# Optimization experiments

Hardware: AMD Instinct MI355X
Metric: run time of the kernel (lower is better)

The kernel has to match this reference:

```python
import jax, jax.numpy as jnp
import numpy as np

K_NBR = 64          # max_num_neighbors in radius()
RATIO1, R1 = 0.5, 0.2
RATIO2, R2 = 0.25, 0.4


def _mlp(h, params):
    # PyG MLP: Linear+ReLU per hidden layer, plain last layer (BN is identity at
    # init / eval with fresh running stats, so omitted).
    for w, b in params[:-1]:
        h = jax.nn.relu(h @ w + b)
    w, b = params[-1]
    return h @ w + b


def _fps(pos, S):
    # Farthest point sampling, deterministic start at index 0. pos: [N,3]
    min_d = jnp.sum((pos - pos[0]) ** 2, axis=-1)

    def body(md, _):
        i = jnp.argmax(md)
        md = jnp.minimum(md, jnp.sum((pos - pos[i]) ** 2, axis=-1))
        return md, i

    _, idxs = jax.lax.scan(body, min_d, None, length=S - 1)
    return jnp.concatenate([jnp.zeros((1,), idxs.dtype), idxs])  # [S]


def _sa(x, pos, S, r, params):
    # One SAModule for a single cloud. x: [N,C], pos: [N,3]
    sel = _fps(pos, S)
    pos_s = pos[sel]                                                   # [S,3]
    d2 = jnp.sum((pos_s[:, None, :] - pos[None, :, :]) ** 2, axis=-1)  # [S,N]
    score = jnp.where(d2 <= r * r, -d2, -jnp.inf)
    vals, nbr = jax.lax.top_k(score, K_NBR)      # <=64 nearest within radius r
    mask = vals > -jnp.inf                       # [S,K]; center always valid
    # PointNetConv message: cat([x_j, pos_j - pos_i]) -> local MLP -> max-aggr
    feats = jnp.concatenate([x[nbr], pos[nbr] - pos_s[:, None, :]], axis=-1)
    h = _mlp(feats, params)                      # [S,K,Cout]
    h = jnp.max(jnp.where(mask[..., None], h, -jnp.inf), axis=1)
    return h, pos_s


def _forward(data, p1, p2, p3, fc_w, fc_b):
    B, N, _ = data.shape
    S1 = int(np.ceil(N * RATIO1))
    S2 = int(np.ceil(S1 * RATIO2))
    # sa1 is called with x = pos = raw coordinates
    x1, pos1 = jax.vmap(lambda p: _sa(p, p, S1, R1, p1))(data)
    x2, pos2 = jax.vmap(lambda x, p: _sa(x, p, S2, R2, p2))(x1, pos1)
    # GlobalSAModule: MLP on cat([x, pos]) then global max pool per cloud
    g = jnp.max(_mlp(jnp.concatenate([x2, pos2], axis=-1), p3), axis=1)  # [B,1024]
    return g @ fc_w + fc_b


def setup_inputs() -> dict:
    key = jax.random.key(0)
    ks = jax.random.split(key, 16)
    B, N = 4, 4096
    inp = {"data": jax.random.uniform(ks[0], (B, N, 3), jnp.float32)}
    dims = {"sa1": [6, 64, 64, 128],
            "sa2": [131, 128, 128, 256],
            "sa3": [259, 256, 512, 1024]}
    i = 1
    for name, ds in dims.items():
        for l in range(len(ds) - 1):
            fi, fo = ds[l], ds[l + 1]
            inp[f"{name}_w{l + 1}"] = (jax.random.normal(ks[i], (fi, fo), jnp.float32)
                                       / np.float32(np.sqrt(fi)))
            inp[f"{name}_b{l + 1}"] = jnp.zeros((fo,), jnp.float32)
            i += 1
    inp["fc_w"] = jax.random.normal(ks[i], (1024, 256), jnp.float32) / np.float32(32.0)
    inp["fc_b"] = jnp.zeros((256,), jnp.float32)
    return inp


def reference(data, sa1_w1, sa1_b1, sa1_w2, sa1_b2, sa1_w3, sa1_b3,
              sa2_w1, sa2_b1, sa2_w2, sa2_b2, sa2_w3, sa2_b3,
              sa3_w1, sa3_b1, sa3_w2, sa3_b2, sa3_w3, sa3_b3,
              fc_w, fc_b):
    p1 = [(sa1_w1, sa1_b1), (sa1_w2, sa1_b2), (sa1_w3, sa1_b3)]
    p2 = [(sa2_w1, sa2_b1), (sa2_w2, sa2_b2), (sa2_w3, sa2_b3)]
    p3 = [(sa3_w1, sa3_b1), (sa3_w2, sa3_b2), (sa3_w3, sa3_b3)]
    return _forward(data, p1, p2, p3, fc_w, fc_b)  # [B, 256]
```

## Files before the change

### kernel.cpp

```cpp
#include <hip/hip_runtime.h>


#define DEVFN __device__ __forceinline__

DEVFN float d2_exact(float ax, float ay, float az, float bx, float by, float bz) {
    float dx = __fsub_rn(ax, bx);
    float dy = __fsub_rn(ay, by);
    float dz = __fsub_rn(az, bz);
    return __fadd_rn(__fadd_rn(__fmul_rn(dx, dx), __fmul_rn(dy, dy)), __fmul_rn(dz, dz));
}

DEVFN unsigned long long u64max(unsigned long long a, unsigned long long b) {
    return a > b ? a : b;
}

template <int R>
DEVFN unsigned long long dpp_ror16_u64(unsigned long long x) {
    int lo = (int)(unsigned)(x & 0xFFFFFFFFull);
    int hi = (int)(unsigned)(x >> 32);
    lo = __builtin_amdgcn_update_dpp(lo, lo, 0x120 | R, 0xF, 0xF, false);
    hi = __builtin_amdgcn_update_dpp(hi, hi, 0x120 | R, 0xF, 0xF, false);
    return ((unsigned long long)(unsigned)hi << 32) | (unsigned)lo;
}

DEVFN unsigned long long rl_u64(unsigned long long x, int lane) {
    unsigned l = (unsigned)__builtin_amdgcn_readlane((int)(unsigned)(x & 0xFFFFFFFFull), lane);
    unsigned h = (unsigned)__builtin_amdgcn_readlane((int)(unsigned)(x >> 32), lane);
    return ((unsigned long long)h << 32) | l;
}

template <int N, int S, int NT>
DEVFN void run_fps(const float* sx, const float* sy, const float* sz,
                   unsigned long long* sPack,
                   int* selLds) {
    constexpr int PPT = N / NT;
    constexpr int NW = NT / 64;
    const int tid = threadIdx.x;
    float px[PPT], py[PPT], pz[PPT], md[PPT];
    unsigned loc[PPT];
#pragma unroll
    for (int i = 0; i < PPT; ++i) {
        int idx = tid * PPT + i;
        px[i] = sx[idx]; py[i] = sy[idx]; pz[i] = sz[idx];
        md[i] = __builtin_inff();
        loc[i] = 0xFFFFFFFFu - (unsigned)idx;
    }
    if (tid == 0) selLds[0] = 0;
    int cur = 0;
    for (int s = 1; s < S; ++s) {
        float ax = sx[cur], ay = sy[cur], az = sz[cur];
        unsigned long long tq[PPT];
#pragma unroll
        for (int i = 0; i < PPT; ++i) {
            float d = d2_exact(px[i], py[i], pz[i], ax, ay, az);
            float m = fminf(md[i], d);
            md[i] = m;
            tq[i] = ((unsigned long long)__float_as_uint(m) << 32) |
                    (unsigned long long)loc[i];
        }
#pragma unroll
        for (int w = PPT / 2; w >= 1; w >>= 1)
#pragma unroll
            for (int i = 0; i < w; ++i) tq[i] = u64max(tq[i], tq[i + w]);

        unsigned long long pk = tq[0];
        pk = u64max(pk, dpp_ror16_u64<8>(pk));
        pk = u64max(pk, dpp_ror16_u64<4>(pk));
        pk = u64max(pk, dpp_ror16_u64<2>(pk));
        pk = u64max(pk, dpp_ror16_u64<1>(pk));

        unsigned long long wmax = u64max(u64max(rl_u64(pk, 0), rl_u64(pk, 16)),
                                         u64max(rl_u64(pk, 32), rl_u64(pk, 48)));

        unsigned long long* sp = sPack + (s & 1) * NW;
        if ((tid & 63) == 0) sp[tid >> 6] = wmax;
        __syncthreads();

        unsigned long long win;
        if constexpr (NW == 8) {
            const ulonglong2* sp2 = (const ulonglong2*)sp;
            ulonglong2 q0 = sp2[0], q1 = sp2[1], q2 = sp2[2], q3 = sp2[3];
            unsigned long long m01 = u64max(u64max(q0.x, q0.y), u64max(q1.x, q1.y));
            unsigned long long m23 = u64max(u64max(q2.x, q2.y), u64max(q3.x, q3.y));
            win = u64max(m01, m23);
        } else {
            const ulonglong2* sp2 = (const ulonglong2*)sp;
            ulonglong2 q0 = sp2[0], q1 = sp2[1];
            win = u64max(u64max(q0.x, q0.y), u64max(q1.x, q1.y));
        }

        cur = (int)(0xFFFFFFFFu - (unsigned)(win & 0xFFFFFFFFull));
        if (tid == 0) selLds[s] = cur;
    }
}

template <int N, int CAP>
DEVFN void nbr_body(const float* __restrict__ pos,
                    const float cx, const float cy, const float cz,
                    const float rsq, const int c,
                    int* __restrict__ nbr, int* __restrict__ cnt,
                    float* sDw, int* sIw) {
    const int lane = threadIdx.x & 63;
    int count = 0;
    for (int j = lane; j < N; j += 64) {
        float d = d2_exact(cx, cy, cz, pos[j * 3 + 0], pos[j * 3 + 1], pos[j * 3 + 2]);
        bool pred = (d <= rsq);
        unsigned long long m = __ballot(pred);
        int wpos = count + __popcll(m & ((1ull << lane) - 1ull));
        if (pred && wpos < CAP) { sDw[wpos] = d; sIw[wpos] = j; }
        count += __popcll(m);
    }
    if (count > CAP) count = CAP;

    for (int t = lane; t < count; t += 64) {
        float d = sDw[t]; int id = sIw[t];
        int rank = 0;
        int j0 = 0;
        for (; j0 + 4 <= count; j0 += 4) {
            float4 dj = *(const float4*)&sDw[j0];
            int4   ij = *(const int4*)&sIw[j0];
            rank += (dj.x < d || (dj.x == d && ij.x < id)) ? 1 : 0;
            rank += (dj.y < d || (dj.y == d && ij.y < id)) ? 1 : 0;
            rank += (dj.z < d || (dj.z == d && ij.z < id)) ? 1 : 0;
            rank += (dj.w < d || (dj.w == d && ij.w < id)) ? 1 : 0;
        }
        for (; j0 < count; ++j0) {
            float dj = sDw[j0]; int ij = sIw[j0];
            rank += (dj < d || (dj == d && ij < id)) ? 1 : 0;
        }
        if (rank < 64) nbr[(size_t)c * 64 + rank] = id;
    }
    if (lane == 0) cnt[c] = count < 64 ? count : 64;
}

__global__ __launch_bounds__(512) void fpsnbr_kernel(
    const float* __restrict__ data,
    float* __restrict__ mdG,
    int* __restrict__ selG,
    float* __restrict__ pos1,
    const int sb, const int se,
    const float rsq, int* __restrict__ nbr1, int* __restrict__ cnt1,
    const int s0)
{
    __shared__ __align__(16) char raw[65536];
    const int tid = threadIdx.x;

    if (blockIdx.x >= 4) {
        float* sD = (float*)raw;
        int*   sI = (int*)(raw + 32768);
        const int wid = tid >> 6;
        const int g = (int)(blockIdx.x - 4) * 8 + wid;
        const int b = g >> 9;
        const int s = s0 + (g & 511);
        const int c = b * 2048 + s;
        const float cx = pos1[(size_t)c * 3 + 0];
        const float cy = pos1[(size_t)c * 3 + 1];
        const float cz = pos1[(size_t)c * 3 + 2];
        nbr_body<4096, 1024>(data + (size_t)b * 4096 * 3, cx, cy, cz, rsq, c,
                             nbr1, cnt1, sD + wid * 1024, sI + wid * 1024);
        return;
    }

    constexpr int N = 4096, NT = 512, PPT = N / NT, NW = NT / 64;
    float* sx = (float*)raw;
    float* sy = sx + 4096;
    float* sz = sy + 4096;
    unsigned long long* sPack = (unsigned long long*)(raw + 49152);
    int* sSel = (int*)(raw + 49280);

    const int b = blockIdx.x;
    const float* p = data + (size_t)b * N * 3;
    for (int i = tid; i < N; i += NT) {
        sx[i] = p[i * 3 + 0]; sy[i] = p[i * 3 + 1]; sz[i] = p[i * 3 + 2];
    }
    __syncthreads();

    float px[PPT], py[PPT], pz[PPT], md[PPT];
    const bool first = (sb == 1);
#pragma unroll
    for (int i = 0; i < PPT; ++i) {
        int idx = tid * PPT + i;
        px[i] = sx[idx]; py[i] = sy[idx]; pz[i] = sz[idx];
        md[i] = first ? __builtin_inff() : mdG[(size_t)b * N + idx];
    }
    int cur = first ? 0 : selG[(size_t)b * 2048 + sb - 1];
    if (first && tid == 0) selG[(size_t)b * 2048] = 0;
    const unsigned lob = 0xFFFFFFFFu - (unsigned)(tid * PPT);

    for (int s = sb; s < se; ++s) {
        float ax = sx[cur], ay = sy[cur], az = sz[cur];
        float mm[PPT];
#pragma unroll
        for (int i = 0; i < PPT; ++i) {
            float d = d2_exact(px[i], py[i], pz[i], ax, ay, az);
            float m = fminf(md[i], d);
            md[i] = m; mm[i] = m;
        }
        float a0 = fmaxf(mm[0], mm[4]), a1 = fmaxf(mm[1], mm[5]);
        float a2 = fmaxf(mm[2], mm[6]), a3 = fmaxf(mm[3], mm[7]);
        float b0 = fmaxf(a0, a2), b1 = fmaxf(a1, a3);
        float mloc = fmaxf(b0, b1);
        int li = 7;
#pragma unroll
        for (int i = 6; i >= 0; --i) li = (mm[i] == mloc) ? i : li;

        unsigned long long k0 =
            ((unsigned long long)__float_as_uint(mloc) << 32) |
            (unsigned long long)(lob - (unsigned)li);

        k0 = u64max(k0, dpp_ror16_u64<8>(k0));
        k0 = u64max(k0, dpp_ror16_u64<4>(k0));
        k0 = u64max(k0, dpp_ror16_u64<2>(k0));
        k0 = u64max(k0, dpp_ror16_u64<1>(k0));

        unsigned long long wmax = u64max(u64max(rl_u64(k0, 0), rl_u64(k0, 16)),
                                         u64max(rl_u64(k0, 32), rl_u64(k0, 48)));

        unsigned long long* sp = sPack + (s & 1) * NW;
        if ((tid & 63) == 0) sp[tid >> 6] = wmax;
        __syncthreads();

        const ulonglong2* sp2 = (const ulonglong2*)sp;
        ulonglong2 q0 = sp2[0], q1 = sp2[1], q2 = sp2[2], q3 = sp2[3];
        unsigned long long m01 = u64max(u64max(q0.x, q0.y), u64max(q1.x, q1.y));
        unsigned long long m23 = u64max(u64max(q2.x, q2.y), u64max(q3.x, q3.y));
        unsigned long long win = u64max(m01, m23);

        cur = (int)(0xFFFFFFFFu - (unsigned)(win & 0xFFFFFFFFull));
        if (tid == 0) sSel[s - sb] = cur;
    }
    __syncthreads();

    if (se < 2048) {
#pragma unroll
        for (int i = 0; i < PPT; ++i)
            mdG[(size_t)b * N + tid * PPT + i] = md[i];
    }
    if (tid == 0) selG[(size_t)b * 2048 + se - 1] = cur;

    float* p1 = pos1 + (size_t)b * 2048 * 3;
    const int sb0 = first ? 0 : sb;
    for (int s = sb0 + tid; s < se; s += NT) {
        int idx = (s == 0) ? 0 : sSel[s - sb];
        p1[s * 3 + 0] = sx[idx]; p1[s * 3 + 1] = sy[idx]; p1[s * 3 + 2] = sz[idx];
    }
}

__global__ __launch_bounds__(512) void fps2nbr_kernel(
    const float* __restrict__ data,
    const float* __restrict__ pos1,
    float* __restrict__ pos2,
    const float rsq, int* __restrict__ nbr1, int* __restrict__ cnt1,
    const int s0)
{
    __shared__ __align__(16) char raw[65536];
    const int tid = threadIdx.x;

    if (blockIdx.x >= 4) {
        float* sD = (float*)raw;
        int*   sI = (int*)(raw + 32768);
        const int wid = tid >> 6;
        const int g = (int)(blockIdx.x - 4) * 8 + wid;
        const int b = g >> 9;
        const int s = s0 + (g & 511);
        const int c = b * 2048 + s;
        const float cx = pos1[(size_t)c * 3 + 0];
        const float cy = pos1[(size_t)c * 3 + 1];
        const float cz = pos1[(size_t)c * 3 + 2];
        nbr_body<4096, 1024>(data + (size_t)b * 4096 * 3, cx, cy, cz, rsq, c,
                             nbr1, cnt1, sD + wid * 1024, sI + wid * 1024);
        return;
    }

    float* sx = (float*)raw;
    float* sy = sx + 2048;
    float* sz = sy + 2048;
    int* sSel2 = (int*)(raw + 24576);
    unsigned long long* sPack2 = (unsigned long long*)(raw + 26624);

    const int b = blockIdx.x;
    const float* p1 = pos1 + (size_t)b * 2048 * 3;
    for (int i = tid; i < 2048; i += 512) {
        sx[i] = p1[i * 3 + 0]; sy[i] = p1[i * 3 + 1]; sz[i] = p1[i * 3 + 2];
    }
    __syncthreads();

    run_fps<2048, 512, 512>(sx, sy, sz, sPack2, sSel2);
    __syncthreads();

    float* p2 = pos2 + (size_t)b * 512 * 3;
    {
        int si = sSel2[tid];
        p2[tid * 3 + 0] = sx[si]; p2[tid * 3 + 1] = sy[si]; p2[tid * 3 + 2] = sz[si];
    }
}

DEVFN void tile44_fma(const float* __restrict__ aBase, int aStride,
                      const float* __restrict__ wBase, int wStride,
                      int nk4, float (&acc)[4][4]) {
    for (int k4 = 0; k4 < nk4; ++k4) {
        float a[4][4], w[4][4];
#pragma unroll
        for (int i = 0; i < 4; ++i) {
            float4 t = *(const float4*)(aBase + i * aStride + k4 * 4);
            a[i][0] = t.x; a[i][1] = t.y; a[i][2] = t.z; a[i][3] = t.w;
        }
#pragma unroll
        for (int kk = 0; kk < 4; ++kk) {
            float4 t = *(const float4*)(wBase + (size_t)(k4 * 4 + kk) * wStride);
            w[kk][0] = t.x; w[kk][1] = t.y; w[kk][2] = t.z; w[kk][3] = t.w;
        }
#pragma unroll
        for (int kk = 0; kk < 4; ++kk)
#pragma unroll
            for (int i = 0; i < 4; ++i)
#pragma unroll
                for (int j = 0; j < 4; ++j)
                    acc[i][j] = fmaf(a[i][kk], w[kk][j], acc[i][j]);
    }
}

DEVFN void tile48_fma(const float* __restrict__ aBase, int aStride,
                      const float* __restrict__ wBase, int wStride,
                      int nk4, float (&acc)[4][8]) {
    for (int k4 = 0; k4 < nk4; ++k4) {
        float a[4][4];
#pragma unroll
        for (int i = 0; i < 4; ++i) {
            float4 t = *(const float4*)(aBase + i * aStride + k4 * 4);
            a[i][0] = t.x; a[i][1] = t.y; a[i][2] = t.z; a[i][3] = t.w;
        }
#pragma unroll
        for (int kk = 0; kk < 4; ++kk) {
            float4 t0 = *(const float4*)(wBase + (size_t)(k4 * 4 + kk) * wStride);
            float4 t1 = *(const float4*)(wBase + (size_t)(k4 * 4 + kk) * wStride + 4);
            float w_[8] = {t0.x, t0.y, t0.z, t0.w, t1.x, t1.y, t1.z, t1.w};
#pragma unroll
            for (int i = 0; i < 4; ++i)
#pragma unroll
                for (int j = 0; j < 8; ++j)
                    acc[i][j] = fmaf(a[i][kk], w_[j], acc[i][j]);
        }
    }
}

__global__ __launch_bounds__(256) void mlp1nbr2_kernel(
    const float* __restrict__ pos,
    const float* __restrict__ ctr,
    const int* __restrict__ nbr, const int* __restrict__ cnt,
    const float* __restrict__ w1, const float* __restrict__ b1,
    const float* __restrict__ w2, const float* __restrict__ b2,
    const float* __restrict__ w3, const float* __restrict__ b3,
    float* __restrict__ x1,
    const float* __restrict__ pos1,
    const float* __restrict__ pos2,
    const float rsq2, int* __restrict__ nbr2, int* __restrict__ cnt2)
{
    __shared__ __align__(16) float smem[12288];
    const int tid = threadIdx.x;

    if (blockIdx.x < 512) {
        float* sD = smem;
        int*   sI = (int*)(smem + 6144);
        const int wid = tid >> 6;
        const int c = (int)blockIdx.x * 4 + wid;
        const int b = c >> 9;
        const float cx = pos2[(size_t)c * 3 + 0];
        const float cy = pos2[(size_t)c * 3 + 1];
        const float cz = pos2[(size_t)c * 3 + 2];
        nbr_body<2048, 1536>(pos1 + (size_t)b * 2048 * 3, cx, cy, cz, rsq2, c,
                             nbr2, cnt2, sD + wid * 1536, sI + wid * 1536);
        return;
    }

    float* sFeat = smem;
    float* sH1   = smem + 576;
    float* sH2   = smem + 4928;
    float* sRed  = smem + 9280;

    const int c = blockIdx.x - 512;
    const int b = c >> 11;
    const int valid = cnt[c];

    if (tid < 64) {
        const int r = tid;
        float fx = 0.f, fy = 0.f, fz = 0.f, dx = 0.f, dy = 0.f, dz = 0.f;
        if (r < valid) {
            int j = nbr[(size_t)c * 64 + r];
            const float* pj = pos + ((size_t)b * 4096 + j) * 3;
            fx = pj[0]; fy = pj[1]; fz = pj[2];
            dx = fx - ctr[c * 3 + 0]; dy = fy - ctr[c * 3 + 1]; dz = fz - ctr[c * 3 + 2];
        }
        float* fr = sFeat + r * 9;
        fr[0] = fx; fr[1] = fy; fr[2] = fz; fr[3] = dx; fr[4] = dy; fr[5] = dz;
    }
    __syncthreads();

    {
        const int r = tid & 63, c0 = (tid >> 6) * 16;
        float acc[16];
#pragma unroll
        for (int q = 0; q < 16; ++q) acc[q] = b1[c0 + q];
#pragma unroll
        for (int k = 0; k < 6; ++k) {
            float a = sFeat[r * 9 + k];
#pragma unroll
            for (int q = 0; q < 16; ++q) acc[q] = fmaf(a, w1[k * 64 + c0 + q], acc[q]);
        }
        float* hr = sH1 + r * 68 + c0;
#pragma unroll
        for (int q = 0; q < 16; ++q) hr[q] = fmaxf(acc[q], 0.f);
    }
    __syncthreads();

    {
        const int r0 = (tid >> 4) * 4, c0 = (tid & 15) * 4;
        float acc[4][4];
#pragma unroll
        for (int i = 0; i < 4; ++i)
#pragma unroll
            for (int j = 0; j < 4; ++j) acc[i][j] = b2[c0 + j];
        tile44_fma(sH1 + r0 * 68, 68, w2 + c0, 64, 16, acc);
#pragma unroll
        for (int i = 0; i < 4; ++i)
#pragma unroll
            for (int j = 0; j < 4; ++j)
                sH2[(r0 + i) * 68 + c0 + j] = fmaxf(acc[i][j], 0.f);
    }
    __syncthreads();

    {
        const int r0 = (tid >> 4) * 4, c0 = (tid & 15) * 8;
        float acc[4][8];
#pragma unroll
        for (int i = 0; i < 4; ++i)
#pragma unroll
            for (int j = 0; j < 8; ++j) acc[i][j] = 0.f;
        tile48_fma(sH2 + r0 * 68, 68, w3 + c0, 128, 16, acc);
        float pm[8];
#pragma unroll
        for (int j = 0; j < 8; ++j) pm[j] = -__builtin_inff();
#pragma unroll
        for (int i = 0; i < 4; ++i)
            if (r0 + i < valid)
#pragma unroll
                for (int j = 0; j < 8; ++j) pm[j] = fmaxf(pm[j], acc[i][j]);
#pragma unroll
        for (int j = 0; j < 8; ++j) sRed[(tid >> 4) * 128 + c0 + j] = pm[j];
    }
    __syncthreads();
    if (tid < 128) {
        float m = -__builtin_inff();
#pragma unroll
        for (int g = 0; g < 16; ++g) m = fmaxf(m, sRed[g * 128 + tid]);
        x1[(size_t)c * 128 + tid] = m + b3[tid];
    }
}

__global__ __launch_bounds__(512, 4) void mlp2_kernel(
    const float* __restrict__ x1,
    const float* __restrict__ pos1,
    const float* __restrict__ ctr,
    const int* __restrict__ nbr, const int* __restrict__ cnt,
    const float* __restrict__ w1, const float* __restrict__ b1,
    const float* __restrict__ w2, const float* __restrict__ b2,
    const float* __restrict__ w3, const float* __restrict__ b3,
    float* __restrict__ x2)
{
    __shared__ __align__(16) float sF[64 * 132];
    __shared__ __align__(16) float sH[64 * 132];
    float* sRed = sH;

    const int tid = threadIdx.x;
    const int c = blockIdx.x;
    const int b = c >> 9;
    const int valid = cnt[c];
    const float cx = ctr[c * 3 + 0], cy = ctr[c * 3 + 1], cz = ctr[c * 3 + 2];

    {
        const int r = tid >> 3, t8 = tid & 7;
        float* fr = sF + r * 132;
        if (r < valid) {
            int j = nbr[(size_t)c * 64 + r];
            const float* xp = x1 + ((size_t)b * 2048 + j) * 128;
#pragma unroll
            for (int q = 0; q < 4; ++q) {
                float4 v = *(const float4*)(xp + t8 * 16 + q * 4);
                fr[t8 * 16 + q * 4 + 0] = v.x; fr[t8 * 16 + q * 4 + 1] = v.y;
                fr[t8 * 16 + q * 4 + 2] = v.z; fr[t8 * 16 + q * 4 + 3] = v.w;
            }
            if (t8 == 0) {
                const float* pj = pos1 + ((size_t)b * 2048 + j) * 3;
                fr[128] = pj[0] - cx; fr[129] = pj[1] - cy; fr[130] = pj[2] - cz;
                fr[131] = 0.f;
            }
        } else {
#pragma unroll
            for (int q = 0; q < 16; ++q) fr[t8 * 16 + q] = 0.f;
            if (t8 == 0) { fr[128] = 0.f; fr[129] = 0.f; fr[130] = 0.f; fr[131] = 0.f; }
        }
    }
    __syncthreads();

    const int r0 = (tid >> 5) * 4;
    const int c0 = (tid & 31) * 4;
    const int c8 = (tid & 31) * 8;

    {
        float acc[4][4];
#pragma unroll
        for (int i = 0; i < 4; ++i)
#pragma unroll
            for (int j = 0; j < 4; ++j) acc[i][j] = b1[c0 + j];
        tile44_fma(sF + r0 * 132, 132, w1 + c0, 128, 32, acc);
        for (int k = 128; k < 131; ++k) {
            float4 wv = *(const float4*)(w1 + (size_t)k * 128 + c0);
            float w_[4] = {wv.x, wv.y, wv.z, wv.w};
#pragma unroll
            for (int i = 0; i < 4; ++i) {
                float a = sF[(r0 + i) * 132 + k];
#pragma unroll
                for (int j = 0; j < 4; ++j) acc[i][j] = fmaf(a, w_[j], acc[i][j]);
            }
        }
#pragma unroll
        for (int i = 0; i < 4; ++i)
#pragma unroll
            for (int j = 0; j < 4; ++j)
                sH[(r0 + i) * 132 + c0 + j] = fmaxf(acc[i][j], 0.f);
    }
    __syncthreads();

    {
        float acc[4][4];
#pragma unroll
        for (int i = 0; i < 4; ++i)
#pragma unroll
            for (int j = 0; j < 4; ++j) acc[i][j] = b2[c0 + j];
        tile44_fma(sH + r0 * 132, 132, w2 + c0, 128, 32, acc);
#pragma unroll
        for (int i = 0; i < 4; ++i)
#pragma unroll
            for (int j = 0; j < 4; ++j)
                sF[(r0 + i) * 132 + c0 + j] = fmaxf(acc[i][j], 0.f);
    }
    __syncthreads();

    {
        float acc[4][8];
#pragma unroll
        for (int i = 0; i < 4; ++i)
#pragma unroll
            for (int j = 0; j < 8; ++j) acc[i][j] = 0.f;
        tile48_fma(sF + r0 * 132, 132, w3 + c8, 256, 32, acc);
        float pm[8];
#pragma unroll
        for (int j = 0; j < 8; ++j) pm[j] = -__builtin_inff();
#pragma unroll
        for (int i = 0; i < 4; ++i)
            if (r0 + i < valid)
#pragma unroll
                for (int j = 0; j < 8; ++j) pm[j] = fmaxf(pm[j], acc[i][j]);
#pragma unroll
        for (int j = 0; j < 8; ++j) sRed[(tid >> 5) * 256 + c8 + j] = pm[j];
    }
    __syncthreads();
    if (tid < 256) {
        float m = -__builtin_inff();
#pragma unroll
        for (int g = 0; g < 16; ++g) m = fmaxf(m, sRed[g * 256 + tid]);
        x2[(size_t)c * 256 + tid] = m + b3[tid];
    }
}

__global__ __launch_bounds__(256) void gemm1f_kernel(const float* __restrict__ x2,
                                                     const float* __restrict__ pos2,
                                                     const float* __restrict__ W,
                                                     const float* __restrict__ bias,
                                                     float* __restrict__ C) {
    constexpr int K = 259, Nc = 256;
    __shared__ __align__(16) float sA[64 * 36];
    __shared__ __align__(16) float sB[32 * 68];
    const int tid = threadIdx.x;
    const int row0 = blockIdx.y * 64, col0 = blockIdx.x * 64;
    const int r0 = (tid >> 4) * 4, c0 = (tid & 15) * 4;
    float acc[4][4];
#pragma unroll
    for (int i = 0; i < 4; ++i)
#pragma unroll
        for (int j = 0; j < 4; ++j) acc[i][j] = 0.f;

    for (int kb = 0; kb < K; kb += 32) {
        for (int l = tid; l < 64 * 32; l += 256) {
            int r = l >> 5, k = l & 31;
            int gk = kb + k;
            float av = 0.f;
            if (gk < K) {
                int row = row0 + r;
                av = (gk < 256) ? x2[(size_t)row * 256 + gk]
                                : pos2[row * 3 + (gk - 256)];
            }
            sA[r * 36 + k] = av;
        }
        for (int l = tid; l < 32 * 64; l += 256) {
            int k = l >> 6, cc = l & 63;
            sB[k * 68 + cc] = (kb + k < K) ? W[(size_t)(kb + k) * Nc + col0 + cc] : 0.f;
        }
        __syncthreads();
        tile44_fma(sA + r0 * 36, 36, sB + c0, 68, 8, acc);
        __syncthreads();
    }
#pragma unroll
    for (int i = 0; i < 4; ++i)
#pragma unroll
        for (int j = 0; j < 4; ++j)
            C[(size_t)(row0 + r0 + i) * Nc + col0 + c0 + j] =
                fmaxf(acc[i][j] + bias[col0 + c0 + j], 0.f);
}

__global__ __launch_bounds__(256) void gemm_kernel(const float* __restrict__ A,
                                                   const float* __restrict__ W,
                                                   const float* __restrict__ bias,
                                                   float* __restrict__ C,
                                                   int M, int K, int Nc, int relu) {
    __shared__ __align__(16) float sA[64 * 36];
    __shared__ __align__(16) float sB[32 * 68];
    const int tid = threadIdx.x;
    const int row0 = blockIdx.y * 64, col0 = blockIdx.x * 64;
    const int r0 = (tid >> 4) * 4, c0 = (tid & 15) * 4;
    float acc[4][4];
#pragma unroll
    for (int i = 0; i < 4; ++i)
#pragma unroll
        for (int j = 0; j < 4; ++j) acc[i][j] = 0.f;

    for (int kb = 0; kb < K; kb += 32) {
        for (int l = tid; l < 64 * 32; l += 256) {
            int r = l >> 5, k = l & 31;
            sA[r * 36 + k] = (kb + k < K) ? A[(size_t)(row0 + r) * K + kb + k] : 0.f;
        }
        for (int l = tid; l < 32 * 64; l += 256) {
            int k = l >> 6, cc = l & 63;
            sB[k * 68 + cc] = (kb + k < K) ? W[(size_t)(kb + k) * Nc + col0 + cc] : 0.f;
        }
        __syncthreads();
        tile44_fma(sA + r0 * 36, 36, sB + c0, 68, 8, acc);
        __syncthreads();
    }
#pragma unroll
    for (int i = 0; i < 4; ++i)
#pragma unroll
        for (int j = 0; j < 4; ++j) {
            float v = acc[i][j] + bias[col0 + c0 + j];
            if (relu) v = fmaxf(v, 0.f);
            C[(size_t)(row0 + r0 + i) * Nc + col0 + c0 + j] = v;
        }
}

__global__ __launch_bounds__(1024) void mpfc_kernel(const float* __restrict__ h,
                                                    const float* __restrict__ w,
                                                    const float* __restrict__ bias,
                                                    float* __restrict__ out) {
    __shared__ float sG[1024];
    __shared__ float sP[4][256];
    const int b = blockIdx.x, tid = threadIdx.x;

    float m = -__builtin_inff();
    const float* hp = h + (size_t)b * 512 * 1024 + tid;
    for (int r = 0; r < 512; ++r) m = fmaxf(m, hp[(size_t)r * 1024]);
    sG[tid] = m;
    __syncthreads();

    const int c = tid & 255, kc = tid >> 8;
    float acc = 0.f;
    const float* wp = w + (size_t)(kc * 256) * 256 + c;
    const float* gp = sG + kc * 256;
    for (int k = 0; k < 256; ++k) acc = fmaf(gp[k], wp[(size_t)k * 256], acc);
    sP[kc][c] = acc;
    __syncthreads();
    if (tid < 256)
        out[b * 256 + tid] = ((sP[0][tid] + sP[1][tid]) + (sP[2][tid] + sP[3][tid]))
                             + bias[tid];
}

extern "C" void kernel_launch(void* const* d_in, const int* in_sizes, int n_in,
                              void* d_out, int out_size, void* d_ws, size_t ws_size,
                              hipStream_t stream) {
    const float* data  = (const float*)d_in[0];
    const float* s1w1  = (const float*)d_in[1];
    const float* s1b1  = (const float*)d_in[2];
    const float* s1w2  = (const float*)d_in[3];
    const float* s1b2  = (const float*)d_in[4];
    const float* s1w3  = (const float*)d_in[5];
    const float* s1b3  = (const float*)d_in[6];
    const float* s2w1  = (const float*)d_in[7];
    const float* s2b1  = (const float*)d_in[8];
    const float* s2w2  = (const float*)d_in[9];
    const float* s2b2  = (const float*)d_in[10];
    const float* s2w3  = (const float*)d_in[11];
    const float* s2b3  = (const float*)d_in[12];
    const float* s3w1  = (const float*)d_in[13];
    const float* s3b1  = (const float*)d_in[14];
    const float* s3w2  = (const float*)d_in[15];
    const float* s3b2  = (const float*)d_in[16];
    const float* s3w3  = (const float*)d_in[17];
    const float* s3b3  = (const float*)d_in[18];
    const float* fcw   = (const float*)d_in[19];
    const float* fcb   = (const float*)d_in[20];
    float* out = (float*)d_out;

    char* ws = (char*)d_ws;
    size_t o = 0;
    auto nxt = [&](size_t bytes) {
        size_t r = o;
        o += (bytes + 255) & ~(size_t)255;
        return r;
    };
    float* pos1 = (float*)(ws + nxt(4 * 2048 * 3 * 4));
    float* pos2 = (float*)(ws + nxt(4 * 512 * 3 * 4));
    float* mdG  = (float*)(ws + nxt(4 * 4096 * 4));
    int*   selG = (int*)(ws + nxt(4 * 2048 * 4));
    int*   nbr1 = (int*)(ws + nxt((size_t)8192 * 64 * 4));
    int*   cnt1 = (int*)(ws + nxt(8192 * 4));
    int*   nbr2 = (int*)(ws + nxt((size_t)2048 * 64 * 4));
    int*   cnt2 = (int*)(ws + nxt(2048 * 4));
    float* x1   = (float*)(ws + nxt((size_t)8192 * 128 * 4));
    float* x2   = (float*)(ws + nxt((size_t)2048 * 256 * 4));
    float* h1   = (float*)(ws + nxt((size_t)2048 * 256 * 4));
    float* h2   = (float*)(ws + nxt((size_t)2048 * 512 * 4));
    float* h3   = (float*)(ws + nxt((size_t)2048 * 1024 * 4));

    const float R1SQ = (float)(0.2 * 0.2);
    const float R2SQ = (float)(0.4 * 0.4);

    fpsnbr_kernel<<<4, 512, 0, stream>>>(data, mdG, selG, pos1, 1, 512,
                                         R1SQ, nbr1, cnt1, 0);
    fpsnbr_kernel<<<260, 512, 0, stream>>>(data, mdG, selG, pos1, 512, 1024,
                                           R1SQ, nbr1, cnt1, 0);
    fpsnbr_kernel<<<260, 512, 0, stream>>>(data, mdG, selG, pos1, 1024, 1536,
                                           R1SQ, nbr1, cnt1, 512);
    fpsnbr_kernel<<<260, 512, 0, stream>>>(data, mdG, selG, pos1, 1536, 2048,
                                           R1SQ, nbr1, cnt1, 1024);
    fps2nbr_kernel<<<260, 512, 0, stream>>>(data, pos1, pos2,
                                            R1SQ, nbr1, cnt1, 1536);
    mlp1nbr2_kernel<<<512 + 8192, 256, 0, stream>>>(data, pos1, nbr1, cnt1,
                                                    s1w1, s1b1, s1w2, s1b2,
                                                    s1w3, s1b3, x1,
                                                    pos1, pos2, R2SQ, nbr2, cnt2);
    mlp2_kernel<<<2048, 512, 0, stream>>>(x1, pos1, pos2, nbr2, cnt2,
                                          s2w1, s2b1, s2w2, s2b2, s2w3, s2b3, x2);
    gemm1f_kernel<<<dim3(4, 32), 256, 0, stream>>>(x2, pos2, s3w1, s3b1, h1);
    gemm_kernel<<<dim3(8, 32), 256, 0, stream>>>(h1, s3w2, s3b2, h2, 2048, 256, 512, 1);
    gemm_kernel<<<dim3(16, 32), 256, 0, stream>>>(h2, s3w3, s3b3, h3, 2048, 512, 1024, 0);
    mpfc_kernel<<<4, 1024, 0, stream>>>(h3, fcw, fcb, out);
}
```

Measured before the change: 2.536 ms.

## Overlap SA1 MLP chunks with later FPS stages via extra blocks

```diff
diff --git a/kernel.cpp b/kernel.cpp
--- a/kernel.cpp
+++ b/kernel.cpp
@@ -133,6 +133,144 @@
     if (lane == 0) cnt[c] = count < 64 ? count : 64;
 }
 
+DEVFN void tile44_fma(const float* __restrict__ aBase, int aStride,
+                      const float* __restrict__ wBase, int wStride,
+                      int nk4, float (&acc)[4][4]) {
+    for (int k4 = 0; k4 < nk4; ++k4) {
+        float a[4][4], w[4][4];
+#pragma unroll
+        for (int i = 0; i < 4; ++i) {
+            float4 t = *(const float4*)(aBase + i * aStride + k4 * 4);
+            a[i][0] = t.x; a[i][1] = t.y; a[i][2] = t.z; a[i][3] = t.w;
+        }
+#pragma unroll
+        for (int kk = 0; kk < 4; ++kk) {
+            float4 t = *(const float4*)(wBase + (size_t)(k4 * 4 + kk) * wStride);
+            w[kk][0] = t.x; w[kk][1] = t.y; w[kk][2] = t.z; w[kk][3] = t.w;
+        }
+#pragma unroll
+        for (int kk = 0; kk < 4; ++kk)
+#pragma unroll
+            for (int i = 0; i < 4; ++i)
+#pragma unroll
+                for (int j = 0; j < 4; ++j)
+                    acc[i][j] = fmaf(a[i][kk], w[kk][j], acc[i][j]);
+    }
+}
+
+DEVFN void tile48_fma(const float* __restrict__ aBase, int aStride,
+                      const float* __restrict__ wBase, int wStride,
+                      int nk4, float (&acc)[4][8]) {
+    for (int k4 = 0; k4 < nk4; ++k4) {
+        float a[4][4];
+#pragma unroll
+        for (int i = 0; i < 4; ++i) {
+            float4 t = *(const float4*)(aBase + i * aStride + k4 * 4);
+            a[i][0] = t.x; a[i][1] = t.y; a[i][2] = t.z; a[i][3] = t.w;
+        }
+#pragma unroll
+        for (int kk = 0; kk < 4; ++kk) {
+            float4 t0 = *(const float4*)(wBase + (size_t)(k4 * 4 + kk) * wStride);
+            float4 t1 = *(const float4*)(wBase + (size_t)(k4 * 4 + kk) * wStride + 4);
+            float w_[8] = {t0.x, t0.y, t0.z, t0.w, t1.x, t1.y, t1.z, t1.w};
+#pragma unroll
+            for (int i = 0; i < 4; ++i)
+#pragma unroll
+                for (int j = 0; j < 8; ++j)
+                    acc[i][j] = fmaf(a[i][kk], w_[j], acc[i][j]);
+        }
+    }
+}
+
+DEVFN void mlp1_body_guarded(const float* __restrict__ pos, const float* __restrict__ ctr,
+                             const int* __restrict__ nbr, const int* __restrict__ cnt,
+                             const float* __restrict__ w1, const float* __restrict__ b1,
+                             const float* __restrict__ w2, const float* __restrict__ b2,
+                             const float* __restrict__ w3, const float* __restrict__ b3,
+                             float* __restrict__ x1, const int c, const int b,
+                             float* smemf) {
+    float* sFeat = smemf;
+    float* sH1   = smemf + 576;
+    float* sH2   = smemf + 4928;
+    float* sRed  = smemf + 9280;
+    const int tid = threadIdx.x;
+    const int valid = cnt[c];
+
+    if (tid < 64) {
+        const int r = tid;
+        float fx = 0.f, fy = 0.f, fz = 0.f, dx = 0.f, dy = 0.f, dz = 0.f;
+        if (r < valid) {
+            int j = nbr[(size_t)c * 64 + r];
+            const float* pj = pos + ((size_t)b * 4096 + j) * 3;
+            fx = pj[0]; fy = pj[1]; fz = pj[2];
+            dx = fx - ctr[c * 3 + 0]; dy = fy - ctr[c * 3 + 1]; dz = fz - ctr[c * 3 + 2];
+        }
+        float* fr = sFeat + r * 9;
+        fr[0] = fx; fr[1] = fy; fr[2] = fz; fr[3] = dx; fr[4] = dy; fr[5] = dz;
+    }
+    __syncthreads();
+
+    if (tid < 256) {
+        const int r = tid & 63, c0 = (tid >> 6) * 16;
+        float acc[16];
+#pragma unroll
+        for (int q = 0; q < 16; ++q) acc[q] = b1[c0 + q];
+#pragma unroll
+        for (int k = 0; k < 6; ++k) {
+            float a = sFeat[r * 9 + k];
+#pragma unroll
+            for (int q = 0; q < 16; ++q) acc[q] = fmaf(a, w1[k * 64 + c0 + q], acc[q]);
+        }
+        float* hr = sH1 + r * 68 + c0;
+#pragma unroll
+        for (int q = 0; q < 16; ++q) hr[q] = fmaxf(acc[q], 0.f);
+    }
+    __syncthreads();
+
+    if (tid < 256) {
+        const int r0 = (tid >> 4) * 4, c0 = (tid & 15) * 4;
+        float acc[4][4];
+#pragma unroll
+        for (int i = 0; i < 4; ++i)
+#pragma unroll
+            for (int j = 0; j < 4; ++j) acc[i][j] = b2[c0 + j];
+        tile44_fma(sH1 + r0 * 68, 68, w2 + c0, 64, 16, acc);
+#pragma unroll
+        for (int i = 0; i < 4; ++i)
+#pragma unroll
+            for (int j = 0; j < 4; ++j)
+                sH2[(r0 + i) * 68 + c0 + j] = fmaxf(acc[i][j], 0.f);
+    }
+    __syncthreads();
+
+    if (tid < 256) {
+        const int r0 = (tid >> 4) * 4, c0 = (tid & 15) * 8;
+        float acc[4][8];
+#pragma unroll
+        for (int i = 0; i < 4; ++i)
+#pragma unroll
+            for (int j = 0; j < 8; ++j) acc[i][j] = 0.f;
+        tile48_fma(sH2 + r0 * 68, 68, w3 + c0, 128, 16, acc);
+        float pm[8];
+#pragma unroll
+        for (int j = 0; j < 8; ++j) pm[j] = -__builtin_inff();
+#pragma unroll
+        for (int i = 0; i < 4; ++i)
+            if (r0 + i < valid)
+#pragma unroll
+                for (int j = 0; j < 8; ++j) pm[j] = fmaxf(pm[j], acc[i][j]);
+#pragma unroll
+        for (int j = 0; j < 8; ++j) sRed[(tid >> 4) * 128 + c0 + j] = pm[j];
+    }
+    __syncthreads();
+    if (tid < 128) {
+        float m = -__builtin_inff();
+#pragma unroll
+        for (int g = 0; g < 16; ++g) m = fmaxf(m, sRed[g * 128 + tid]);
+        x1[(size_t)c * 128 + tid] = m + b3[tid];
+    }
+}
+
 __global__ __launch_bounds__(512) void fpsnbr_kernel(
     const float* __restrict__ data,
     float* __restrict__ mdG,
@@ -140,18 +278,30 @@
     float* __restrict__ pos1,
     const int sb, const int se,
     const float rsq, int* __restrict__ nbr1, int* __restrict__ cnt1,
-    const int s0)
+    const int s0n,
+    const float* __restrict__ w1, const float* __restrict__ b1,
+    const float* __restrict__ w2, const float* __restrict__ b2,
+    const float* __restrict__ w3, const float* __restrict__ b3,
+    float* __restrict__ x1, const int s0m)
 {
     __shared__ __align__(16) char raw[65536];
     const int tid = threadIdx.x;
 
+    if (blockIdx.x >= 260) {
+        const int g = (int)blockIdx.x - 260;
+        const int b = g >> 9;
+        const int c = b * 2048 + s0m + (g & 511);
+        mlp1_body_guarded(data, pos1, nbr1, cnt1, w1, b1, w2, b2, w3, b3,
+                          x1, c, b, (float*)raw);
+        return;
+    }
     if (blockIdx.x >= 4) {
         float* sD = (float*)raw;
         int*   sI = (int*)(raw + 32768);
         const int wid = tid >> 6;
         const int g = (int)(blockIdx.x - 4) * 8 + wid;
         const int b = g >> 9;
-        const int s = s0 + (g & 511);
+        const int s = s0n + (g & 511);
         const int c = b * 2048 + s;
         const float cx = pos1[(size_t)c * 3 + 0];
         const float cy = pos1[(size_t)c * 3 + 1];
@@ -251,18 +401,30 @@
     const float* __restrict__ pos1,
     float* __restrict__ pos2,
     const float rsq, int* __restrict__ nbr1, int* __restrict__ cnt1,
-    const int s0)
+    const int s0n,
+    const float* __restrict__ w1, const float* __restrict__ b1,
+    const float* __restrict__ w2, const float* __restrict__ b2,
+    const float* __restrict__ w3, const float* __restrict__ b3,
+    float* __restrict__ x1, const int s0m)
 {
     __shared__ __align__(16) char raw[65536];
     const int tid = threadIdx.x;
 
+    if (blockIdx.x >= 260) {
+        const int g = (int)blockIdx.x - 260;
+        const int b = g >> 9;
+        const int c = b * 2048 + s0m + (g & 511);
+        mlp1_body_guarded(data, pos1, nbr1, cnt1, w1, b1, w2, b2, w3, b3,
+                          x1, c, b, (float*)raw);
+        return;
+    }
     if (blockIdx.x >= 4) {
         float* sD = (float*)raw;
         int*   sI = (int*)(raw + 32768);
         const int wid = tid >> 6;
         const int g = (int)(blockIdx.x - 4) * 8 + wid;
         const int b = g >> 9;
-        const int s = s0 + (g & 511);
+        const int s = s0n + (g & 511);
         const int c = b * 2048 + s;
         const float cx = pos1[(size_t)c * 3 + 0];
         const float cy = pos1[(size_t)c * 3 + 1];
@@ -292,55 +454,6 @@
     {
         int si = sSel2[tid];
         p2[tid * 3 + 0] = sx[si]; p2[tid * 3 + 1] = sy[si]; p2[tid * 3 + 2] = sz[si];
-    }
-}
-
-DEVFN void tile44_fma(const float* __restrict__ aBase, int aStride,
-                      const float* __restrict__ wBase, int wStride,
-                      int nk4, float (&acc)[4][4]) {
-    for (int k4 = 0; k4 < nk4; ++k4) {
-        float a[4][4], w[4][4];
-#pragma unroll
-        for (int i = 0; i < 4; ++i) {
-            float4 t = *(const float4*)(aBase + i * aStride + k4 * 4);
-            a[i][0] = t.x; a[i][1] = t.y; a[i][2] = t.z; a[i][3] = t.w;
-        }
-#pragma unroll
-        for (int kk = 0; kk < 4; ++kk) {
-            float4 t = *(const float4*)(wBase + (size_t)(k4 * 4 + kk) * wStride);
-            w[kk][0] = t.x; w[kk][1] = t.y; w[kk][2] = t.z; w[kk][3] = t.w;
-        }
-#pragma unroll
-        for (int kk = 0; kk < 4; ++kk)
-#pragma unroll
-            for (int i = 0; i < 4; ++i)
-#pragma unroll
-                for (int j = 0; j < 4; ++j)
-                    acc[i][j] = fmaf(a[i][kk], w[kk][j], acc[i][j]);
-    }
-}
-
-DEVFN void tile48_fma(const float* __restrict__ aBase, int aStride,
-                      const float* __restrict__ wBase, int wStride,
-                      int nk4, float (&acc)[4][8]) {
-    for (int k4 = 0; k4 < nk4; ++k4) {
-        float a[4][4];
-#pragma unroll
-        for (int i = 0; i < 4; ++i) {
-            float4 t = *(const float4*)(aBase + i * aStride + k4 * 4);
-            a[i][0] = t.x; a[i][1] = t.y; a[i][2] = t.z; a[i][3] = t.w;
-        }
-#pragma unroll
-        for (int kk = 0; kk < 4; ++kk) {
-            float4 t0 = *(const float4*)(wBase + (size_t)(k4 * 4 + kk) * wStride);
-            float4 t1 = *(const float4*)(wBase + (size_t)(k4 * 4 + kk) * wStride + 4);
-            float w_[8] = {t0.x, t0.y, t0.z, t0.w, t1.x, t1.y, t1.z, t1.w};
-#pragma unroll
-            for (int i = 0; i < 4; ++i)
-#pragma unroll
-                for (int j = 0; j < 8; ++j)
-                    acc[i][j] = fmaf(a[i][kk], w_[j], acc[i][j]);
-        }
     }
 }
 
@@ -354,7 +467,8 @@
     float* __restrict__ x1,
     const float* __restrict__ pos1,
     const float* __restrict__ pos2,
-    const float rsq2, int* __restrict__ nbr2, int* __restrict__ cnt2)
+    const float rsq2, int* __restrict__ nbr2, int* __restrict__ cnt2,
+    const int s0m)
 {
     __shared__ __align__(16) float smem[12288];
     const int tid = threadIdx.x;
@@ -373,88 +487,11 @@
         return;
     }
 
-    float* sFeat = smem;
-    float* sH1   = smem + 576;
-    float* sH2   = smem + 4928;
-    float* sRed  = smem + 9280;
-
-    const int c = blockIdx.x - 512;
-    const int b = c >> 11;
-    const int valid = cnt[c];
-
-    if (tid < 64) {
-        const int r = tid;
-        float fx = 0.f, fy = 0.f, fz = 0.f, dx = 0.f, dy = 0.f, dz = 0.f;
-        if (r < valid) {
-            int j = nbr[(size_t)c * 64 + r];
-            const float* pj = pos + ((size_t)b * 4096 + j) * 3;
-            fx = pj[0]; fy = pj[1]; fz = pj[2];
-            dx = fx - ctr[c * 3 + 0]; dy = fy - ctr[c * 3 + 1]; dz = fz - ctr[c * 3 + 2];
-        }
-        float* fr = sFeat + r * 9;
-        fr[0] = fx; fr[1] = fy; fr[2] = fz; fr[3] = dx; fr[4] = dy; fr[5] = dz;
-    }
-    __syncthreads();
-
-    {
-        const int r = tid & 63, c0 = (tid >> 6) * 16;
-        float acc[16];
-#pragma unroll
-        for (int q = 0; q < 16; ++q) acc[q] = b1[c0 + q];
-#pragma unroll
-        for (int k = 0; k < 6; ++k) {
-            float a = sFeat[r * 9 + k];
-#pragma unroll
-            for (int q = 0; q < 16; ++q) acc[q] = fmaf(a, w1[k * 64 + c0 + q], acc[q]);
-        }
-        float* hr = sH1 + r * 68 + c0;
-#pragma unroll
-        for (int q = 0; q < 16; ++q) hr[q] = fmaxf(acc[q], 0.f);
-    }
-    __syncthreads();
-
-    {
-        const int r0 = (tid >> 4) * 4, c0 = (tid & 15) * 4;
-        float acc[4][4];
-#pragma unroll
-        for (int i = 0; i < 4; ++i)
-#pragma unroll
-            for (int j = 0; j < 4; ++j) acc[i][j] = b2[c0 + j];
-        tile44_fma(sH1 + r0 * 68, 68, w2 + c0, 64, 16, acc);
-#pragma unroll
-        for (int i = 0; i < 4; ++i)
-#pragma unroll
-            for (int j = 0; j < 4; ++j)
-                sH2[(r0 + i) * 68 + c0 + j] = fmaxf(acc[i][j], 0.f);
-    }
-    __syncthreads();
-
-    {
-        const int r0 = (tid >> 4) * 4, c0 = (tid & 15) * 8;
-        float acc[4][8];
-#pragma unroll
-        for (int i = 0; i < 4; ++i)
-#pragma unroll
-            for (int j = 0; j < 8; ++j) acc[i][j] = 0.f;
-        tile48_fma(sH2 + r0 * 68, 68, w3 + c0, 128, 16, acc);
-        float pm[8];
-#pragma unroll
-        for (int j = 0; j < 8; ++j) pm[j] = -__builtin_inff();
-#pragma unroll
-        for (int i = 0; i < 4; ++i)
-            if (r0 + i < valid)
-#pragma unroll
-                for (int j = 0; j < 8; ++j) pm[j] = fmaxf(pm[j], acc[i][j]);
-#pragma unroll
-        for (int j = 0; j < 8; ++j) sRed[(tid >> 4) * 128 + c0 + j] = pm[j];
-    }
-    __syncthreads();
-    if (tid < 128) {
-        float m = -__builtin_inff();
-#pragma unroll
-        for (int g = 0; g < 16; ++g) m = fmaxf(m, sRed[g * 128 + tid]);
-        x1[(size_t)c * 128 + tid] = m + b3[tid];
-    }
+    const int g = (int)blockIdx.x - 512;
+    const int b = g >> 9;
+    const int c = b * 2048 + s0m + (g & 511);
+    mlp1_body_guarded(pos, ctr, nbr, cnt, w1, b1, w2, b2, w3, b3,
+                      x1, c, b, smem);
 }
 
 __global__ __launch_bounds__(512, 4) void mlp2_kernel(
@@ -734,19 +771,24 @@
     const float R2SQ = (float)(0.4 * 0.4);
 
     fpsnbr_kernel<<<4, 512, 0, stream>>>(data, mdG, selG, pos1, 1, 512,
-                                         R1SQ, nbr1, cnt1, 0);
+                                         R1SQ, nbr1, cnt1, 0,
+                                         s1w1, s1b1, s1w2, s1b2, s1w3, s1b3, x1, 0);
     fpsnbr_kernel<<<260, 512, 0, stream>>>(data, mdG, selG, pos1, 512, 1024,
-                                           R1SQ, nbr1, cnt1, 0);
-    fpsnbr_kernel<<<260, 512, 0, stream>>>(data, mdG, selG, pos1, 1024, 1536,
-                                           R1SQ, nbr1, cnt1, 512);
-    fpsnbr_kernel<<<260, 512, 0, stream>>>(data, mdG, selG, pos1, 1536, 2048,
-                                           R1SQ, nbr1, cnt1, 1024);
-    fps2nbr_kernel<<<260, 512, 0, stream>>>(data, pos1, pos2,
-                                            R1SQ, nbr1, cnt1, 1536);
-    mlp1nbr2_kernel<<<512 + 8192, 256, 0, stream>>>(data, pos1, nbr1, cnt1,
-                                                    s1w1, s1b1, s1w2, s1b2,
-                                                    s1w3, s1b3, x1,
-                                                    pos1, pos2, R2SQ, nbr2, cnt2);
+                                           R1SQ, nbr1, cnt1, 0,
+                                           s1w1, s1b1, s1w2, s1b2, s1w3, s1b3, x1, 0);
+    fpsnbr_kernel<<<2308, 512, 0, stream>>>(data, mdG, selG, pos1, 1024, 1536,
+                                            R1SQ, nbr1, cnt1, 512,
+                                            s1w1, s1b1, s1w2, s1b2, s1w3, s1b3, x1, 0);
+    fpsnbr_kernel<<<2308, 512, 0, stream>>>(data, mdG, selG, pos1, 1536, 2048,
+                                            R1SQ, nbr1, cnt1, 1024,
+                                            s1w1, s1b1, s1w2, s1b2, s1w3, s1b3, x1, 512);
+    fps2nbr_kernel<<<2308, 512, 0, stream>>>(data, pos1, pos2,
+                                             R1SQ, nbr1, cnt1, 1536,
+                                             s1w1, s1b1, s1w2, s1b2, s1w3, s1b3, x1, 1024);
+    mlp1nbr2_kernel<<<2560, 256, 0, stream>>>(data, pos1, nbr1, cnt1,
+                                              s1w1, s1b1, s1w2, s1b2,
+                                              s1w3, s1b3, x1,
+                                              pos1, pos2, R2SQ, nbr2, cnt2, 1536);
     mlp2_kernel<<<2048, 512, 0, stream>>>(x1, pos1, pos2, nbr2, cnt2,
                                           s2w1, s2b1, s2w2, s2b2, s2w3, s2b3, x2);
     gemm1f_kernel<<<dim3(4, 32), 256, 0, stream>>>(x2, pos2, s3w1, s3b1, h1);
```

After: 2.467 ms. -2.7%, faster.
